# Performance work log

Hardware: AMD Instinct MI355X
Metric: run time of the kernel (lower is better)

The kernel has to match this reference:

```python
import jax, jax.numpy as jnp
import numpy as np

N_USER = 100000
M_ITEM = 50000
N_NODE = N_USER + M_ITEM
D = 64           # latent_dim
WD = D // 2      # word_emb_dim
FU = FI = 10     # padded feature-bag width
NUF = NIF = 30000
VOCAB = 20000
T = 8            # tokens per text source (name/comment/comment_list)
DNU = DNI = 10   # numeric feature dims
B = 2048         # seed batch
S = 20           # sampled neighbors per layer
L = 2            # num_layers


def setup_inputs() -> dict:
    key = jax.random.key(0)
    ks = jax.random.split(key, 26)
    f = lambda i, s: jax.random.normal(ks[i], s, jnp.float32) * 0.05
    ri = lambda i, s, hi: jax.random.randint(ks[i], s, 0, hi)
    return {
        # int (graph / lookup) inputs
        "seeds": ri(0, (B,), N_USER),
        "neigh1": ri(1, (B, S), N_NODE),
        "neigh2": ri(2, (B, S, S), N_NODE),
        "user_feat_idx": ri(3, (N_USER, FU), NUF),
        "item_feat_idx": ri(4, (M_ITEM, FI), NIF),
        "user_text_idx": ri(5, (N_USER, 3, T), VOCAB),
        "item_text_idx": ri(6, (M_ITEM, 3, T), VOCAB),
        # float tables / features
        "user_id_emb": f(7, (N_USER, D)),
        "item_id_emb": f(8, (M_ITEM, D)),
        "user_feat_emb": f(9, (NUF, D)),
        "item_feat_emb": f(10, (NIF, D)),
        "word_emb": f(11, (VOCAB, WD)),
        "user_word300": f(12, (N_USER, 300)),
        "item_word300": f(13, (M_ITEM, 300)),
        "item_sent768": f(14, (M_ITEM, 768)),
        "user_numeric": f(15, (N_USER, DNU)),
        "item_numeric": f(16, (M_ITEM, DNI)),
        # linears (stored as (in, out); y = x @ W + b)
        "Wnum_u": f(17, (DNU, D)), "bnum_u": jnp.zeros((D,), jnp.float32),
        "Wnum_i": f(18, (DNI, D)), "bnum_i": jnp.zeros((D,), jnp.float32),
        "Wproj_u": f(19, (int(D * 3.5) + 300, D)), "bproj_u": jnp.zeros((D,), jnp.float32),
        "Wproj_i": f(20, (int(D * 3.5) + 300 + 768, D)), "bproj_i": jnp.zeros((D,), jnp.float32),
        "W_w": f(21, (L, 2 * D, D)), "b_w": jnp.zeros((L, D), jnp.float32),
        "W_v": f(22, (L, D, D)), "b_v": jnp.zeros((L, D), jnp.float32),
    }


def _forward(user_id_emb, item_id_emb, user_feat_emb, item_feat_emb, word_emb,
             user_word300, item_word300, item_sent768, user_numeric, item_numeric,
             Wnum_u, bnum_u, Wnum_i, bnum_i, Wproj_u, bproj_u, Wproj_i, bproj_i,
             W_w, b_w, W_v, b_v,
             seeds, neigh1, neigh2, user_feat_idx, item_feat_idx,
             user_text_idx, item_text_idx):
    # --- multi-source node embeddings (get_text_embedding + proj + numeric) ---
    # text: mean-pool word embeddings per source, concat 3 sources -> 1.5*D
    u_text = word_emb[user_text_idx].mean(axis=2).reshape(N_USER, 3 * WD)
    i_text = word_emb[item_text_idx].mean(axis=2).reshape(M_ITEM, 3 * WD)
    # feature bags: mean-pooled embedding lookup
    u_feat = user_feat_emb[user_feat_idx].mean(axis=1)
    i_feat = item_feat_emb[item_feat_idx].mean(axis=1)
    u = (jnp.concatenate([user_id_emb, u_feat, u_text, user_word300], -1) @ Wproj_u
         + bproj_u + user_numeric @ Wnum_u + bnum_u)
    it = (jnp.concatenate([item_id_emb, i_feat, i_text, item_word300, item_sent768], -1) @ Wproj_i
          + bproj_i + item_numeric @ Wnum_i + bnum_i)
    x = jnp.concatenate([u, it], axis=0)  # [N_NODE, D], items offset by N_USER

    # --- neighbor-sampled GraphSAGE: h = W_l([self, mean(V_l(neigh))]) ---
    def sage(l, self_x, neigh_x, act):
        agg = (neigh_x @ W_v[l] + b_v[l]).mean(axis=-2)
        h = jnp.concatenate([self_x, agg], axis=-1) @ W_w[l] + b_w[l]
        return jax.nn.relu(h) if act else h

    x0 = x[seeds]        # [B, D]
    x1 = x[neigh1]       # [B, S, D]
    x2 = x[neigh2]       # [B, S, S, D]
    h1 = sage(0, x1, x2, True)   # layer-0 applied to 1-hop nodes
    h0 = sage(0, x0, x1, True)   # layer-0 applied to seeds
    out = sage(1, h0, h1, False)  # final layer, no activation
    return out  # [B, D]


def reference(seeds, neigh1, neigh2, user_feat_idx, item_feat_idx, user_text_idx,
              item_text_idx, user_id_emb, item_id_emb, user_feat_emb, item_feat_emb,
              word_emb, user_word300, item_word300, item_sent768, user_numeric,
              item_numeric, Wnum_u, bnum_u, Wnum_i, bnum_i, Wproj_u, bproj_u,
              Wproj_i, bproj_i, W_w, b_w, W_v, b_v):
    return _forward(user_id_emb, item_id_emb, user_feat_emb, item_feat_emb, word_emb,
                    user_word300, item_word300, item_sent768, user_numeric, item_numeric,
                    Wnum_u, bnum_u, Wnum_i, bnum_i, Wproj_u, bproj_u, Wproj_i, bproj_i,
                    W_w, b_w, W_v, b_v,
                    seeds, neigh1, neigh2, user_feat_idx, item_feat_idx,
                    user_text_idx, item_text_idx)
```

## Files before the change

kernel.cpp:

```cpp
#include <hip/hip_runtime.h>
#include <hip/hip_bf16.h>
#include <stdint.h>

#define N_USER 100000
#define M_ITEM 50000
#define N_NODE 150000
#define B_SEED 2048
#define S_NB 20
#define UBLK2 1563
#define IBLK2 782

typedef __bf16   bf16x8 __attribute__((ext_vector_type(8)));
typedef float    f32x4  __attribute__((ext_vector_type(4)));
typedef uint32_t u32x4  __attribute__((ext_vector_type(4)));

typedef __attribute__((address_space(3))) uint32_t lds_u32_t;
typedef __attribute__((address_space(1))) const uint32_t glb_u32_t;

__device__ __forceinline__ uint16_t f2bf(float f) {
    uint32_t u = __float_as_uint(f);
    return (uint16_t)((u + 0x7FFFu + ((u >> 16) & 1u)) >> 16);
}
__device__ __forceinline__ uint32_t pk2(float a, float b) {
    __hip_bfloat162 h = __float22bfloat162_rn(make_float2(a, b));
    return *reinterpret_cast<uint32_t*>(&h);
}
__device__ __forceinline__ float bf2f(uint16_t u) {
    return __uint_as_float(((uint32_t)u) << 16);
}

union BF8 { bf16x8 v; uint32_t u[4]; };

__device__ __forceinline__ bf16x8 pack8v(f32x4 lo, f32x4 hi) {
    BF8 r;
    r.u[0] = pk2(lo[0], lo[1]); r.u[1] = pk2(lo[2], lo[3]);
    r.u[2] = pk2(hi[0], hi[1]); r.u[3] = pk2(hi[2], hi[3]);
    return r.v;
}
__device__ __forceinline__ bf16x8 ldf32x8_mask(const float* rowp, int base, int limit) {
    BF8 r;
#pragma unroll
    for (int h = 0; h < 4; ++h) {
        const int k0 = base + 2 * h;
        const float a = (k0     < limit) ? rowp[k0]     : 0.f;
        const float b = (k0 + 1 < limit) ? rowp[k0 + 1] : 0.f;
        r.u[h] = pk2(a, b);
    }
    return r.v;
}

__global__ void prep_kernel(const float* __restrict__ Wproj_u, const float* __restrict__ Wnum_u,
                            const float* __restrict__ Wproj_i, const float* __restrict__ Wnum_i,
                            const float* __restrict__ Wv0, const float* __restrict__ Ww0,
                            uint16_t* __restrict__ WTU, uint16_t* __restrict__ WTI,
                            uint16_t* __restrict__ WvT, uint16_t* __restrict__ WwT)
{
    const int idx = blockIdx.x * 256 + threadIdx.x;
    if (idx < 36864) {
        const int d = idx / 576, kp = idx - d * 576;
        float v = 0.f;
        if (kp < 160)      v = Wproj_u[(64 + kp) * 64 + d];
        else if (kp < 192) { const int j = kp - 160; if (j < 10) v = Wnum_u[j * 64 + d]; }
        else if (kp < 224) { const int j = kp - 192; if (j < 12) v = Wproj_u[(512 + j) * 64 + d]; }
        else if (kp < 288) v = Wproj_u[(kp - 224) * 64 + d];
        else               v = Wproj_u[(224 + kp - 288) * 64 + d];
        WTU[d * 576 + kp] = f2bf(v);
    } else if (idx < 122880) {
        const int i2 = idx - 36864;
        const int d = i2 / 1344, kp = i2 - d * 1344;
        float v = 0.f;
        if (kp < 160)      v = Wproj_i[(64 + kp) * 64 + d];
        else if (kp < 192) { const int j = kp - 160; if (j < 10) v = Wnum_i[j * 64 + d]; }
        else if (kp < 224) { const int j = kp - 192; if (j < 12) v = Wproj_i[(512 + j) * 64 + d]; }
        else if (kp < 288) v = Wproj_i[(kp - 224) * 64 + d];
        else if (kp < 576) v = Wproj_i[(224 + kp - 288) * 64 + d];
        else               v = Wproj_i[(524 + kp - 576) * 64 + d];
        WTI[d * 1344 + kp] = f2bf(v);
    } else {
        const int i2 = idx - 122880;
        if (i2 < 4096) { const int d = i2 >> 6, k = i2 & 63;  WvT[d * 64 + k]  = f2bf(Wv0[k * 64 + d]); }
        else           { const int j = i2 - 4096;
                         const int d = j >> 7, k = j & 127;   WwT[d * 128 + k] = f2bf(Ww0[k * 64 + d]); }
    }
}

__global__ __launch_bounds__(256) void gpack_kernel(
    const int* __restrict__ ufi, const int* __restrict__ ifi,
    const int* __restrict__ uti, const int* __restrict__ iti,
    const float* __restrict__ ufe, const float* __restrict__ ife,
    const float* __restrict__ wemb,
    uint16_t* __restrict__ Apre)
{
    const int gid  = blockIdx.x * 256 + threadIdx.x;
    const int node = gid >> 3;
    const int d0   = gid & 7;
    if (node >= N_NODE) return;
    const bool item = node >= N_USER;
    const int nloc  = item ? node - N_USER : node;
    const int*   fidx = (item ? ifi : ufi) + (size_t)nloc * 10;
    const int*   tidx = (item ? iti : uti) + (size_t)nloc * 24;
    const float* fe   = item ? ife : ufe;
    uint16_t* out = Apre + (size_t)node * 160;

    {
        f32x4 s0 = {0, 0, 0, 0}, s1 = {0, 0, 0, 0};
#pragma unroll
        for (int j = 0; j < 10; ++j) {
            const float* p = fe + (size_t)fidx[j] * 64 + 8 * d0;
            s0 += *(const f32x4*)p;
            s1 += *(const f32x4*)(p + 4);
        }
        s0 *= 0.1f; s1 *= 0.1f;
        uint4 o = make_uint4(pk2(s0[0], s0[1]), pk2(s0[2], s0[3]),
                             pk2(s1[0], s1[1]), pk2(s1[2], s1[3]));
        *(uint4*)(out + 8 * d0) = o;
    }
#pragma unroll
    for (int s = 0; s < 3; ++s) {
        f32x4 a = {0, 0, 0, 0};
#pragma unroll
        for (int j = 0; j < 8; ++j) {
            const float* p = wemb + (size_t)tidx[s * 8 + j] * 32 + 4 * d0;
            a += *(const f32x4*)p;
        }
        a *= 0.125f;
        *(uint2*)(out + 64 + 32 * s + 4 * d0) = make_uint2(pk2(a[0], a[1]), pk2(a[2], a[3]));
    }
}

__global__ __launch_bounds__(256, 6) void pgemm_kernel(
    const uint16_t* __restrict__ Apre,
    const float* __restrict__ u_id,  const float* __restrict__ i_id,
    const float* __restrict__ uw300, const float* __restrict__ iw300,
    const float* __restrict__ is768,
    const float* __restrict__ unum,  const float* __restrict__ inum,
    const uint16_t* __restrict__ WTU, const uint16_t* __restrict__ WTI,
    const float* __restrict__ bproj_u, const float* __restrict__ bnum_u,
    const float* __restrict__ bproj_i, const float* __restrict__ bnum_i,
    uint16_t* __restrict__ xout)
{
    __shared__ float buf[2][4096];

    const int t = threadIdx.x;
    const int w = t >> 6, l = t & 63;
    const int l15 = l & 15, g4 = l >> 4;
    const bool item = blockIdx.x < IBLK2;
    const int tile  = item ? blockIdx.x : (blockIdx.x - IBLK2);
    const int ntype = item ? M_ITEM : N_USER;
    const int nb    = tile * 64;
    const int NC    = item ? 17 : 5;

    const float* idp = item ? i_id  : u_id;
    const float* w3p = item ? iw300 : uw300;
    const float* nmp = item ? inum  : unum;
    const uint16_t* WT = item ? WTI : WTU;
    const int KP       = item ? 1344 : 576;

    f32x4 acc[4] = {};
    const uint16_t* WTb = WT + (size_t)l15 * KP + g4 * 8;

    auto MM = [&](bf16x8 af2, int kb) {
#pragma unroll
        for (int db = 0; db < 4; ++db) {
            const bf16x8 bfr = *reinterpret_cast<const bf16x8*>(WTb + (size_t)db * 16 * KP + kb);
            acc[db] = __builtin_amdgcn_mfma_f32_16x16x32_bf16(af2, bfr, acc[db], 0, 0, 0);
        }
    };

    auto stage = [&](int bi, int c) {
        const float* base; int stride, coloff;
        if (c == 0)      { base = idp;   stride = 64;  coloff = 0; }
        else if (c < 5)  { base = w3p;   stride = 300; coloff = (c - 1) * 64; }
        else             { base = is768; stride = 768; coloff = (c - 5) * 64; }
        char* wbase = (char*)&buf[bi][0] + w * 4096;
#pragma unroll
        for (int j = 0; j < 4; ++j) {
            const int row  = j * 4 + (l >> 4);
            const int nn   = nb + w * 16 + row;
            const int node = nn < ntype ? nn : (ntype - 1);
            const int swb  = ((l & 15) * 16) ^ ((row & 7) << 4);
            const float* g = base + (size_t)node * stride + coloff + (swb >> 2);
            __builtin_amdgcn_global_load_lds((glb_u32_t*)g,
                (lds_u32_t*)(void*)(wbase + j * 1024), 16, 0, 0);
        }
    };

    auto compute = [&](int bi, int kb0) {
        const char* wbase = (const char*)&buf[bi][0] + w * 4096;
        const int r = l15;
#pragma unroll
        for (int ks = 0; ks < 2; ++ks) {
            const f32x4 lo = *(const f32x4*)(wbase + r * 256 + ((ks * 128 + g4 * 32)      ^ ((r & 7) << 4)));
            const f32x4 hi = *(const f32x4*)(wbase + r * 256 + ((ks * 128 + g4 * 32 + 16) ^ ((r & 7) << 4)));
            MM(pack8v(lo, hi), kb0 + ks * 32);
        }
    };

    const int nloc = (nb + w * 16 + l15) < ntype ? (nb + w * 16 + l15) : (ntype - 1);
    const int node = (item ? N_USER : 0) + nloc;
    const uint16_t* ap = Apre + (size_t)node * 160 + g4 * 8;
    bf16x8 af[5];
#pragma unroll
    for (int ks = 0; ks < 5; ++ks) af[ks] = *(const bf16x8*)(ap + ks * 32);
    const float* wr = w3p + (size_t)nloc * 300;
    const bf16x8 numf  = ldf32x8_mask(nmp + (size_t)nloc * 10, g4 * 8, 10);
    const bf16x8 tailf = ldf32x8_mask(wr, 288 + g4 * 8, 300);
    const bf16x8 w300c = pack8v(*(const f32x4*)(wr + 256 + g4 * 8),
                                *(const f32x4*)(wr + 260 + g4 * 8));

    stage(0, 0);
#pragma unroll
    for (int ks = 0; ks < 5; ++ks) MM(af[ks], ks * 32);
    MM(numf, 160);
    MM(tailf, 192);
    MM(w300c, 544);

    for (int c = 0; c < NC; ++c) {
        if (c + 1 < NC) stage((c + 1) & 1, c + 1);
        __syncthreads();
        compute(c & 1, (c < 5) ? 224 + 64 * c : 576 + 64 * (c - 5));
        __syncthreads();
    }

    const int nb_out = nb + w * 16 + g4 * 4;
    const float* bp = item ? bproj_i : bproj_u;
    const float* bn = item ? bnum_i  : bnum_u;
    uint16_t* xo = xout + (size_t)(item ? N_USER : 0) * 64;
#pragma unroll
    for (int db = 0; db < 4; ++db) {
        const int d = db * 16 + l15;
        const float bias = bp[d] + bn[d];
#pragma unroll
        for (int r = 0; r < 4; ++r) {
            const int nn = nb_out + r;
            if (nn < ntype) xo[(size_t)nn * 64 + d] = f2bf(acc[db][r] + bias);
        }
    }
}

__global__ __launch_bounds__(256) void xv_kernel(
    const uint16_t* __restrict__ x, const uint16_t* __restrict__ WvT,
    const float* __restrict__ bv, uint16_t* __restrict__ xv, int n)
{
    const int t = threadIdx.x;
    const int w = t >> 6, l = t & 63, l15 = l & 15, g4 = l >> 4;
    const int node = blockIdx.x * 64 + w * 16 + l15;
    const int node_c = node < n ? node : n - 1;

    f32x4 acc[4] = {};
    const uint16_t* WTb = WvT + l15 * 64 + g4 * 8;
#pragma unroll
    for (int ks = 0; ks < 2; ++ks) {
        const bf16x8 af = *reinterpret_cast<const bf16x8*>(x + (size_t)node_c * 64 + ks * 32 + g4 * 8);
#pragma unroll
        for (int db = 0; db < 4; ++db) {
            const bf16x8 bfr = *reinterpret_cast<const bf16x8*>(WTb + db * 16 * 64 + ks * 32);
            acc[db] = __builtin_amdgcn_mfma_f32_16x16x32_bf16(af, bfr, acc[db], 0, 0, 0);
        }
    }
    const int node_base = blockIdx.x * 64 + w * 16 + g4 * 4;
#pragma unroll
    for (int db = 0; db < 4; ++db) {
        const int d = db * 16 + l15;
        const float bias = bv[d];
#pragma unroll
        for (int r = 0; r < 4; ++r) {
            const int nn = node_base + r;
            if (nn < n) xv[(size_t)nn * 64 + d] = f2bf(acc[db][r] + bias);
        }
    }
}

__global__ __launch_bounds__(256) void sage_fused_kernel(
    const uint16_t* __restrict__ x, const uint16_t* __restrict__ xv,
    const int* __restrict__ seeds, const int* __restrict__ neigh1,
    const int* __restrict__ neigh2,
    const uint16_t* __restrict__ WwT, const float* __restrict__ bw,
    uint16_t* __restrict__ h1, uint16_t* __restrict__ h0)
{
    const int t = threadIdx.x;
    const int w = t >> 6, l = t & 63, l15 = l & 15, g4 = l >> 4;
    const int rbase = blockIdx.x * 64 + w * 16;
    const bool is1 = rbase < 40960;
    const int r = rbase + l15;
    const int sidx = is1 ? neigh1[r] : seeds[r - 40960];
    const int* ni = is1 ? (neigh2 + (size_t)r * S_NB)
                        : (neigh1 + (size_t)(r - 40960) * S_NB);

    f32x4 acc[4] = {};
    const uint16_t* WTb = WwT + l15 * 128 + g4 * 8;

    auto MM = [&](bf16x8 af, int kb) {
#pragma unroll
        for (int db = 0; db < 4; ++db) {
            const bf16x8 bfr = *reinterpret_cast<const bf16x8*>(WTb + db * 16 * 128 + kb);
            acc[db] = __builtin_amdgcn_mfma_f32_16x16x32_bf16(af, bfr, acc[db], 0, 0, 0);
        }
    };

#pragma unroll
    for (int ks = 0; ks < 2; ++ks) {
        const bf16x8 af = *reinterpret_cast<const bf16x8*>(x + (size_t)sidx * 64 + ks * 32 + g4 * 8);
        MM(af, ks * 32);
    }
#pragma unroll
    for (int ks = 0; ks < 2; ++ks) {
        float ev[4] = {0.f, 0.f, 0.f, 0.f}, od[4] = {0.f, 0.f, 0.f, 0.f};
#pragma unroll
        for (int j = 0; j < S_NB; ++j) {
            const u32x4 v = *reinterpret_cast<const u32x4*>(xv + (size_t)ni[j] * 64 + ks * 32 + g4 * 8);
#pragma unroll
            for (int q = 0; q < 4; ++q) {
                ev[q] += __uint_as_float(v[q] << 16);
                od[q] += __uint_as_float(v[q] & 0xffff0000u);
            }
        }
        BF8 m;
#pragma unroll
        for (int q = 0; q < 4; ++q) m.u[q] = pk2(ev[q] * (1.f / S_NB), od[q] * (1.f / S_NB));
        MM(m.v, 64 + ks * 32);
    }

    const int rb = blockIdx.x * 64 + w * 16 + g4 * 4;
    uint16_t* ob = is1 ? h1 : h0;
    const int rowoff = is1 ? 0 : 40960;
#pragma unroll
    for (int db = 0; db < 4; ++db) {
        const int d = db * 16 + l15;
        const float bias = bw[d];
#pragma unroll
        for (int rr = 0; rr < 4; ++rr) {
            const float h = fmaxf(acc[db][rr] + bias, 0.f);
            ob[(size_t)(rb + rr - rowoff) * 64 + d] = f2bf(h);
        }
    }
}

__global__ __launch_bounds__(256) void final_kernel(
    const uint16_t* __restrict__ h0, const uint16_t* __restrict__ h1,
    const float* __restrict__ Wv, const float* __restrict__ bv,
    const float* __restrict__ Ww, const float* __restrict__ bw,
    float* __restrict__ out)
{
    __shared__ float WvL[64 * 64];
    __shared__ float WwL[128 * 64];
    const int t = threadIdx.x;
    for (int i = t; i < 64 * 64; i += 256)  WvL[i] = Wv[i];
    for (int i = t; i < 128 * 64; i += 256) WwL[i] = Ww[i];
    __syncthreads();

    const int wave = t >> 6, lane = t & 63;
    const int base = blockIdx.x * 32 + wave * 8;
    const float bvl = bv[lane], bwl = bw[lane];

    for (int i = 0; i < 8; ++i) {
        const int b = base + i;
        float m = 0.f;
#pragma unroll
        for (int s = 0; s < S_NB; ++s)
            m += bf2f(h1[(size_t)(b * S_NB + s) * 64 + lane]);
        m *= (1.f / S_NB);

        float agg = bvl;
#pragma unroll 8
        for (int k = 0; k < 64; ++k)
            agg += __shfl(m, k) * WvL[k * 64 + lane];

        const float selfv = bf2f(h0[(size_t)b * 64 + lane]);
        float h = bwl;
#pragma unroll 8
        for (int k = 0; k < 64; ++k)
            h += __shfl(selfv, k) * WwL[k * 64 + lane];
#pragma unroll 8
        for (int k = 0; k < 64; ++k)
            h += __shfl(agg, k) * WwL[(64 + k) * 64 + lane];

        out[(size_t)b * 64 + lane] = h;
    }
}

extern "C" void kernel_launch(void* const* d_in, const int* in_sizes, int n_in,
                              void* d_out, int out_size, void* d_ws, size_t ws_size,
                              hipStream_t stream)
{
    const int*   seeds   = (const int*)d_in[0];
    const int*   neigh1  = (const int*)d_in[1];
    const int*   neigh2  = (const int*)d_in[2];
    const int*   ufi     = (const int*)d_in[3];
    const int*   ifi     = (const int*)d_in[4];
    const int*   uti     = (const int*)d_in[5];
    const int*   iti     = (const int*)d_in[6];
    const float* u_id    = (const float*)d_in[7];
    const float* i_id    = (const float*)d_in[8];
    const float* ufe     = (const float*)d_in[9];
    const float* ife     = (const float*)d_in[10];
    const float* wemb    = (const float*)d_in[11];
    const float* uw300   = (const float*)d_in[12];
    const float* iw300   = (const float*)d_in[13];
    const float* is768   = (const float*)d_in[14];
    const float* unum    = (const float*)d_in[15];
    const float* inum    = (const float*)d_in[16];
    const float* Wnum_u  = (const float*)d_in[17];
    const float* bnum_u  = (const float*)d_in[18];
    const float* Wnum_i  = (const float*)d_in[19];
    const float* bnum_i  = (const float*)d_in[20];
    const float* Wproj_u = (const float*)d_in[21];
    const float* bproj_u = (const float*)d_in[22];
    const float* Wproj_i = (const float*)d_in[23];
    const float* bproj_i = (const float*)d_in[24];
    const float* W_w     = (const float*)d_in[25];
    const float* b_w     = (const float*)d_in[26];
    const float* W_v     = (const float*)d_in[27];
    const float* b_v     = (const float*)d_in[28];

    uint16_t* WTU  = (uint16_t*)d_ws;
    uint16_t* WTI  = WTU  + 36864;
    uint16_t* WvT0 = WTI  + 86016;
    uint16_t* WwT0 = WvT0 + 4096;
    uint16_t* xbf  = WwT0 + 8192;
    uint16_t* xvbf = xbf  + (size_t)N_NODE * 64;
    uint16_t* h1bf = xvbf + (size_t)N_NODE * 64;
    uint16_t* h0bf = h1bf + (size_t)B_SEED * S_NB * 64;
    uint16_t* Apre = xvbf;
    float* outp = (float*)d_out;

    prep_kernel<<<528, 256, 0, stream>>>(
        Wproj_u, Wnum_u, Wproj_i, Wnum_i, W_v, W_w, WTU, WTI, WvT0, WwT0);

    gpack_kernel<<<(N_NODE * 8 + 255) / 256, 256, 0, stream>>>(
        ufi, ifi, uti, iti, ufe, ife, wemb, Apre);

    pgemm_kernel<<<UBLK2 + IBLK2, 256, 0, stream>>>(
        Apre, u_id, i_id, uw300, iw300, is768, unum, inum,
        WTU, WTI, bproj_u, bnum_u, bproj_i, bnum_i, xbf);

    xv_kernel<<<(N_NODE + 63) / 64, 256, 0, stream>>>(xbf, WvT0, b_v, xvbf, N_NODE);

    sage_fused_kernel<<<672, 256, 0, stream>>>(
        xbf, xvbf, seeds, neigh1, neigh2, WwT0, b_w, h1bf, h0bf);

    final_kernel<<<B_SEED / 32, 256, 0, stream>>>(
        h0bf, h1bf, W_v + 4096, b_v + 64, W_w + 8192, b_w + 64, outp);
}
```

Before: 340.2 us.

## Halve pgemm tile to 32 nodes with 32-column chunks and register-prefetched weights

The projection GEMM now runs 128-thread blocks covering 32 nodes instead of 256-thread blocks covering 64. The K dimension is streamed in 32-float chunks rather than 64, so the LDS staging buffer shrinks, more blocks can be resident, and the launch grid roughly doubles. The weight fragments for the next chunk are preloaded into registers alongside the async LDS stage, and the loop is manually double-buffered. The separate handling of columns 256–287 of the 300-wide features is folded into the regular chunk stream. The cost is twice as many barrier-separated iterations, each doing less work.

```diff
diff --git a/kernel.cpp b/kernel.cpp
--- a/kernel.cpp
+++ b/kernel.cpp
@@ -7,8 +7,8 @@
 #define N_NODE 150000
 #define B_SEED 2048
 #define S_NB 20
-#define UBLK2 1563
-#define IBLK2 782
+#define UBLK3 3125
+#define IBLK3 1563
 
 typedef __bf16   bf16x8 __attribute__((ext_vector_type(8)));
 typedef float    f32x4  __attribute__((ext_vector_type(4)));
@@ -128,7 +128,7 @@
     }
 }
 
-__global__ __launch_bounds__(256, 6) void pgemm_kernel(
+__global__ __launch_bounds__(128, 7) void pgemm_kernel(
     const uint16_t* __restrict__ Apre,
     const float* __restrict__ u_id,  const float* __restrict__ i_id,
     const float* __restrict__ uw300, const float* __restrict__ iw300,
@@ -139,16 +139,17 @@
     const float* __restrict__ bproj_i, const float* __restrict__ bnum_i,
     uint16_t* __restrict__ xout)
 {
-    __shared__ float buf[2][4096];
+    __shared__ float buf[2][1024];
 
     const int t = threadIdx.x;
-    const int w = t >> 6, l = t & 63;
+    const int w = t >> 6;
+    const int l = t & 63;
     const int l15 = l & 15, g4 = l >> 4;
-    const bool item = blockIdx.x < IBLK2;
-    const int tile  = item ? blockIdx.x : (blockIdx.x - IBLK2);
+    const bool item = blockIdx.x < IBLK3;
+    const int tile  = item ? blockIdx.x : (blockIdx.x - IBLK3);
     const int ntype = item ? M_ITEM : N_USER;
-    const int nb    = tile * 64;
-    const int NC    = item ? 17 : 5;
+    const int nb    = tile * 32;
+    const int NC    = item ? 35 : 11;
 
     const float* idp = item ? i_id  : u_id;
     const float* w3p = item ? iw300 : uw300;
@@ -169,58 +170,69 @@
 
     auto stage = [&](int bi, int c) {
         const float* base; int stride, coloff;
-        if (c == 0)      { base = idp;   stride = 64;  coloff = 0; }
-        else if (c < 5)  { base = w3p;   stride = 300; coloff = (c - 1) * 64; }
-        else             { base = is768; stride = 768; coloff = (c - 5) * 64; }
-        char* wbase = (char*)&buf[bi][0] + w * 4096;
-#pragma unroll
-        for (int j = 0; j < 4; ++j) {
-            const int row  = j * 4 + (l >> 4);
-            const int nn   = nb + w * 16 + row;
+        if (c < 2)       { base = idp;    stride = 64;  coloff = c * 32; }
+        else if (c < 11) { base = w3p;    stride = 300; coloff = (c - 2) * 32; }
+        else             { base = is768;  stride = 768; coloff = (c - 11) * 32; }
+        char* wbase = (char*)&buf[bi][0] + w * 2048;
+#pragma unroll
+        for (int j = 0; j < 2; ++j) {
+            const int rl   = j * 8 + (l >> 3);
+            const int nn   = nb + w * 16 + rl;
             const int node = nn < ntype ? nn : (ntype - 1);
-            const int swb  = ((l & 15) * 16) ^ ((row & 7) << 4);
+            const int swb  = ((l & 7) * 16) ^ ((rl & 7) << 4);
             const float* g = base + (size_t)node * stride + coloff + (swb >> 2);
             __builtin_amdgcn_global_load_lds((glb_u32_t*)g,
                 (lds_u32_t*)(void*)(wbase + j * 1024), 16, 0, 0);
         }
     };
 
-    auto compute = [&](int bi, int kb0) {
-        const char* wbase = (const char*)&buf[bi][0] + w * 4096;
+    auto loadB = [&](bf16x8* breg, int c) {
+        const int kb = 224 + 32 * c;
+#pragma unroll
+        for (int i = 0; i < 4; ++i)
+            breg[i] = *reinterpret_cast<const bf16x8*>(WTb + (size_t)i * 16 * KP + kb);
+    };
+
+    auto computeR = [&](int bi, const bf16x8* breg) {
+        const char* wbase = (const char*)&buf[bi][0] + w * 2048;
         const int r = l15;
-#pragma unroll
-        for (int ks = 0; ks < 2; ++ks) {
-            const f32x4 lo = *(const f32x4*)(wbase + r * 256 + ((ks * 128 + g4 * 32)      ^ ((r & 7) << 4)));
-            const f32x4 hi = *(const f32x4*)(wbase + r * 256 + ((ks * 128 + g4 * 32 + 16) ^ ((r & 7) << 4)));
-            MM(pack8v(lo, hi), kb0 + ks * 32);
-        }
+        const f32x4 lo = *(const f32x4*)(wbase + r * 128 + ((g4 * 32)      ^ ((r & 7) << 4)));
+        const f32x4 hi = *(const f32x4*)(wbase + r * 128 + ((g4 * 32 + 16) ^ ((r & 7) << 4)));
+        const bf16x8 af2 = pack8v(lo, hi);
+#pragma unroll
+        for (int db = 0; db < 4; ++db)
+            acc[db] = __builtin_amdgcn_mfma_f32_16x16x32_bf16(af2, breg[db], acc[db], 0, 0, 0);
     };
 
+    stage(0, 0);
     const int nloc = (nb + w * 16 + l15) < ntype ? (nb + w * 16 + l15) : (ntype - 1);
     const int node = (item ? N_USER : 0) + nloc;
-    const uint16_t* ap = Apre + (size_t)node * 160 + g4 * 8;
-    bf16x8 af[5];
-#pragma unroll
-    for (int ks = 0; ks < 5; ++ks) af[ks] = *(const bf16x8*)(ap + ks * 32);
-    const float* wr = w3p + (size_t)nloc * 300;
-    const bf16x8 numf  = ldf32x8_mask(nmp + (size_t)nloc * 10, g4 * 8, 10);
-    const bf16x8 tailf = ldf32x8_mask(wr, 288 + g4 * 8, 300);
-    const bf16x8 w300c = pack8v(*(const f32x4*)(wr + 256 + g4 * 8),
-                                *(const f32x4*)(wr + 260 + g4 * 8));
-
-    stage(0, 0);
-#pragma unroll
-    for (int ks = 0; ks < 5; ++ks) MM(af[ks], ks * 32);
-    MM(numf, 160);
-    MM(tailf, 192);
-    MM(w300c, 544);
-
-    for (int c = 0; c < NC; ++c) {
-        if (c + 1 < NC) stage((c + 1) & 1, c + 1);
+    {
+        const uint16_t* ap = Apre + (size_t)node * 160 + g4 * 8;
+        bf16x8 af[5];
+#pragma unroll
+        for (int ks = 0; ks < 5; ++ks) af[ks] = *(const bf16x8*)(ap + ks * 32);
+        const bf16x8 numf  = ldf32x8_mask(nmp + (size_t)nloc * 10, g4 * 8, 10);
+        const bf16x8 tailf = ldf32x8_mask(w3p + (size_t)nloc * 300, 288 + g4 * 8, 300);
+#pragma unroll
+        for (int ks = 0; ks < 5; ++ks) MM(af[ks], ks * 32);
+        MM(numf, 160);
+        MM(tailf, 192);
+    }
+
+    bf16x8 bA[4], bB[4];
+    loadB(bA, 0);
+    int c = 0;
+#pragma unroll 1
+    for (; c + 2 <= NC; c += 2) {
+        stage(1, c + 1); loadB(bB, c + 1);
         __syncthreads();
-        compute(c & 1, (c < 5) ? 224 + 64 * c : 576 + 64 * (c - 5));
+        computeR(0, bA);
+        if (c + 2 < NC) { stage(0, c + 2); loadB(bA, c + 2); }
         __syncthreads();
-    }
+        computeR(1, bB);
+    }
+    if (c < NC) computeR(0, bA);
 
     const int nb_out = nb + w * 16 + g4 * 4;
     const float* bp = item ? bproj_i : bproj_u;
@@ -430,7 +442,7 @@
     gpack_kernel<<<(N_NODE * 8 + 255) / 256, 256, 0, stream>>>(
         ufi, ifi, uti, iti, ufe, ife, wemb, Apre);
 
-    pgemm_kernel<<<UBLK2 + IBLK2, 256, 0, stream>>>(
+    pgemm_kernel<<<UBLK3 + IBLK3, 128, 0, stream>>>(
         Apre, u_id, i_id, uw300, iw300, is768, unum, inum,
         WTU, WTI, bproj_u, bnum_u, bproj_i, bnum_i, xbf);
 
```

After: 370.2 us. 1.09x slower.

## Pre-pack full projection operand into swizzled bf16 tiles for async LDS GEMM

Applied to the files above, without the earlier changes.

The gather/pack kernel now writes the whole projection A operand for each node into a tile-major, XOR-swizzled bf16 layout of 128 rows by 64 columns per chunk. That operand covers id embeddings, word300, sent768, numeric and text features. The GEMM kernel then streams these chunks straight into LDS with global_load_lds. It handles 128 rows per block, and users and items are launched as separate kernels. The aim is to remove the fp32-to-bf16 conversion and the strided fp32 row gathers from the GEMM inner loop. The cost is a large extra write and read of the packed intermediate, plus a much bigger workspace footprint.

```diff
diff --git a/kernel.cpp b/kernel.cpp
--- a/kernel.cpp
+++ b/kernel.cpp
@@ -7,8 +7,10 @@
 #define N_NODE 150000
 #define B_SEED 2048
 #define S_NB 20
-#define UBLK2 1563
-#define IBLK2 782
+#define TILES_U 782
+#define TILES_I 391
+#define NCH_U 9
+#define NCH_I 21
 
 typedef __bf16   bf16x8 __attribute__((ext_vector_type(8)));
 typedef float    f32x4  __attribute__((ext_vector_type(4)));
@@ -31,22 +33,17 @@
 
 union BF8 { bf16x8 v; uint32_t u[4]; };
 
-__device__ __forceinline__ bf16x8 pack8v(f32x4 lo, f32x4 hi) {
-    BF8 r;
-    r.u[0] = pk2(lo[0], lo[1]); r.u[1] = pk2(lo[2], lo[3]);
-    r.u[2] = pk2(hi[0], hi[1]); r.u[3] = pk2(hi[2], hi[3]);
-    return r.v;
-}
-__device__ __forceinline__ bf16x8 ldf32x8_mask(const float* rowp, int base, int limit) {
-    BF8 r;
-#pragma unroll
-    for (int h = 0; h < 4; ++h) {
-        const int k0 = base + 2 * h;
-        const float a = (k0     < limit) ? rowp[k0]     : 0.f;
-        const float b = (k0 + 1 < limit) ? rowp[k0 + 1] : 0.f;
-        r.u[h] = pk2(a, b);
-    }
-    return r.v;
+__device__ __forceinline__ uint4 packrow(const float* p) {
+    const f32x4 a = *(const f32x4*)p, b = *(const f32x4*)(p + 4);
+    return make_uint4(pk2(a[0], a[1]), pk2(a[2], a[3]),
+                      pk2(b[0], b[1]), pk2(b[2], b[3]));
+}
+__device__ __forceinline__ uint4 maskrow(const float* p, int j0, int lim) {
+    float v[8];
+#pragma unroll
+    for (int h = 0; h < 8; ++h) v[h] = (j0 + h < lim) ? p[j0 + h] : 0.f;
+    return make_uint4(pk2(v[0], v[1]), pk2(v[2], v[3]),
+                      pk2(v[4], v[5]), pk2(v[6], v[7]));
 }
 
 __global__ void prep_kernel(const float* __restrict__ Wproj_u, const float* __restrict__ Wnum_u,
@@ -84,23 +81,28 @@
     }
 }
 
+template<int IS_ITEM>
 __global__ __launch_bounds__(256) void gpack_kernel(
-    const int* __restrict__ ufi, const int* __restrict__ ifi,
-    const int* __restrict__ uti, const int* __restrict__ iti,
-    const float* __restrict__ ufe, const float* __restrict__ ife,
-    const float* __restrict__ wemb,
-    uint16_t* __restrict__ Apre)
-{
+    const int* __restrict__ fidx_, const int* __restrict__ tidx_,
+    const float* __restrict__ fe, const float* __restrict__ wemb,
+    const float* __restrict__ idt, const float* __restrict__ w3t,
+    const float* __restrict__ s7t, const float* __restrict__ nmt,
+    uint16_t* __restrict__ Apack)
+{
+    constexpr int NTYPE = IS_ITEM ? M_ITEM : N_USER;
+    constexpr int NCH   = IS_ITEM ? NCH_I : NCH_U;
     const int gid  = blockIdx.x * 256 + threadIdx.x;
     const int node = gid >> 3;
     const int d0   = gid & 7;
-    if (node >= N_NODE) return;
-    const bool item = node >= N_USER;
-    const int nloc  = item ? node - N_USER : node;
-    const int*   fidx = (item ? ifi : ufi) + (size_t)nloc * 10;
-    const int*   tidx = (item ? iti : uti) + (size_t)nloc * 24;
-    const float* fe   = item ? ife : ufe;
-    uint16_t* out = Apre + (size_t)node * 160;
+    if (node >= NTYPE) return;
+    const int tile = node >> 7, r = node & 127, w = r >> 5, r32 = r & 31;
+    char* out = (char*)Apack + (size_t)tile * NCH * 16384 + w * 4096
+              + r32 * 128 + ((d0 * 16) ^ ((r32 & 7) << 4));
+
+    const int* fidx = fidx_ + (size_t)node * 10;
+    const int* tidx = tidx_ + (size_t)node * 24;
+    const float* wr  = w3t + (size_t)node * 300;
+    const float* idr = idt + (size_t)node * 64;
 
     {
         f32x4 s0 = {0, 0, 0, 0}, s1 = {0, 0, 0, 0};
@@ -111,129 +113,110 @@
             s1 += *(const f32x4*)(p + 4);
         }
         s0 *= 0.1f; s1 *= 0.1f;
-        uint4 o = make_uint4(pk2(s0[0], s0[1]), pk2(s0[2], s0[3]),
-                             pk2(s1[0], s1[1]), pk2(s1[2], s1[3]));
-        *(uint4*)(out + 8 * d0) = o;
-    }
-#pragma unroll
-    for (int s = 0; s < 3; ++s) {
-        f32x4 a = {0, 0, 0, 0};
+        *(uint4*)out = make_uint4(pk2(s0[0], s0[1]), pk2(s0[2], s0[3]),
+                                  pk2(s1[0], s1[1]), pk2(s1[2], s1[3]));
+    }
+    auto text8 = [&](int src, int dd) -> uint4 {
+        f32x4 a = {0, 0, 0, 0}, b = {0, 0, 0, 0};
 #pragma unroll
         for (int j = 0; j < 8; ++j) {
-            const float* p = wemb + (size_t)tidx[s * 8 + j] * 32 + 4 * d0;
+            const float* p = wemb + (size_t)tidx[src * 8 + j] * 32 + dd;
             a += *(const f32x4*)p;
-        }
-        a *= 0.125f;
-        *(uint2*)(out + 64 + 32 * s + 4 * d0) = make_uint2(pk2(a[0], a[1]), pk2(a[2], a[3]));
-    }
-}
-
-__global__ __launch_bounds__(256, 6) void pgemm_kernel(
-    const uint16_t* __restrict__ Apre,
-    const float* __restrict__ u_id,  const float* __restrict__ i_id,
-    const float* __restrict__ uw300, const float* __restrict__ iw300,
-    const float* __restrict__ is768,
-    const float* __restrict__ unum,  const float* __restrict__ inum,
-    const uint16_t* __restrict__ WTU, const uint16_t* __restrict__ WTI,
-    const float* __restrict__ bproj_u, const float* __restrict__ bnum_u,
-    const float* __restrict__ bproj_i, const float* __restrict__ bnum_i,
-    uint16_t* __restrict__ xout)
-{
-    __shared__ float buf[2][4096];
+            b += *(const f32x4*)(p + 4);
+        }
+        a *= 0.125f; b *= 0.125f;
+        return make_uint4(pk2(a[0], a[1]), pk2(a[2], a[3]),
+                          pk2(b[0], b[1]), pk2(b[2], b[3]));
+    };
+    *(uint4*)(out + 16384) = text8(d0 >> 2, (d0 & 3) * 8);
+    *(uint4*)(out + 2 * 16384) = (d0 < 4)
+        ? text8(2, d0 * 8)
+        : maskrow(nmt + (size_t)node * 10, (d0 - 4) * 8, 10);
+    *(uint4*)(out + 3 * 16384) = (d0 < 4)
+        ? maskrow(wr + 288, d0 * 8, 12)
+        : packrow(idr + (d0 - 4) * 8);
+    *(uint4*)(out + 4 * 16384) = (d0 < 4)
+        ? packrow(idr + 32 + d0 * 8)
+        : packrow(wr + (d0 - 4) * 8);
+#pragma unroll
+    for (int c = 5; c < 9; ++c)
+        *(uint4*)(out + c * 16384) = packrow(wr + c * 64 + d0 * 8 - 288);
+    if (IS_ITEM) {
+        const float* sr = s7t + (size_t)node * 768;
+#pragma unroll
+        for (int c = 9; c < 21; ++c)
+            *(uint4*)(out + c * 16384) = packrow(sr + c * 64 + d0 * 8 - 576);
+    }
+}
+
+__global__ __launch_bounds__(256, 4) void pgemm3_kernel(
+    const uint16_t* __restrict__ Apack, const uint16_t* __restrict__ WT,
+    const float* __restrict__ bp, const float* __restrict__ bn,
+    uint16_t* __restrict__ xout, int ntype, int nch, int KP)
+{
+    __shared__ char lds[2][16384];
 
     const int t = threadIdx.x;
     const int w = t >> 6, l = t & 63;
     const int l15 = l & 15, g4 = l >> 4;
-    const bool item = blockIdx.x < IBLK2;
-    const int tile  = item ? blockIdx.x : (blockIdx.x - IBLK2);
-    const int ntype = item ? M_ITEM : N_USER;
-    const int nb    = tile * 64;
-    const int NC    = item ? 17 : 5;
-
-    const float* idp = item ? i_id  : u_id;
-    const float* w3p = item ? iw300 : uw300;
-    const float* nmp = item ? inum  : unum;
-    const uint16_t* WT = item ? WTI : WTU;
-    const int KP       = item ? 1344 : 576;
-
-    f32x4 acc[4] = {};
+    const int nb = blockIdx.x * 128;
+
+    f32x4 acc[2][4] = {};
     const uint16_t* WTb = WT + (size_t)l15 * KP + g4 * 8;
-
-    auto MM = [&](bf16x8 af2, int kb) {
+    const char* Atile = (const char*)Apack + (size_t)blockIdx.x * nch * 16384;
+
+    auto stage = [&](int bi, int c) {
+        const char* src = Atile + c * 16384 + w * 4096 + l * 16;
+        char* dst = &lds[bi][w * 4096];
+#pragma unroll
+        for (int j = 0; j < 4; ++j)
+            __builtin_amdgcn_global_load_lds((glb_u32_t*)(src + j * 1024),
+                (lds_u32_t*)(void*)(dst + j * 1024), 16, 0, 0);
+    };
+
+    auto compute = [&](int bi, int c) {
+        const char* wb = &lds[bi][w * 4096];
+#pragma unroll
+        for (int ks = 0; ks < 2; ++ks) {
+            bf16x8 bfr[4];
+#pragma unroll
+            for (int db = 0; db < 4; ++db)
+                bfr[db] = *reinterpret_cast<const bf16x8*>(
+                    WTb + (size_t)db * 16 * KP + c * 64 + ks * 32);
+#pragma unroll
+            for (int frag = 0; frag < 2; ++frag) {
+                const int r32 = frag * 16 + l15;
+                const bf16x8 af = *(const bf16x8*)(wb + r32 * 128
+                    + ((ks * 64 + g4 * 16) ^ ((r32 & 7) << 4)));
+#pragma unroll
+                for (int db = 0; db < 4; ++db)
+                    acc[frag][db] = __builtin_amdgcn_mfma_f32_16x16x32_bf16(
+                        af, bfr[db], acc[frag][db], 0, 0, 0);
+            }
+        }
+    };
+
+    stage(0, 0);
+#pragma unroll 1
+    for (int c = 0; c < nch; ++c) {
+        if (c + 1 < nch) stage((c + 1) & 1, c + 1);
+        __syncthreads();
+        compute(c & 1, c);
+        __syncthreads();
+    }
+
+#pragma unroll
+    for (int frag = 0; frag < 2; ++frag) {
+        const int rb = nb + w * 32 + frag * 16 + g4 * 4;
 #pragma unroll
         for (int db = 0; db < 4; ++db) {
-            const bf16x8 bfr = *reinterpret_cast<const bf16x8*>(WTb + (size_t)db * 16 * KP + kb);
-            acc[db] = __builtin_amdgcn_mfma_f32_16x16x32_bf16(af2, bfr, acc[db], 0, 0, 0);
-        }
-    };
-
-    auto stage = [&](int bi, int c) {
-        const float* base; int stride, coloff;
-        if (c == 0)      { base = idp;   stride = 64;  coloff = 0; }
-        else if (c < 5)  { base = w3p;   stride = 300; coloff = (c - 1) * 64; }
-        else             { base = is768; stride = 768; coloff = (c - 5) * 64; }
-        char* wbase = (char*)&buf[bi][0] + w * 4096;
-#pragma unroll
-        for (int j = 0; j < 4; ++j) {
-            const int row  = j * 4 + (l >> 4);
-            const int nn   = nb + w * 16 + row;
-            const int node = nn < ntype ? nn : (ntype - 1);
-            const int swb  = ((l & 15) * 16) ^ ((row & 7) << 4);
-            const float* g = base + (size_t)node * stride + coloff + (swb >> 2);
-            __builtin_amdgcn_global_load_lds((glb_u32_t*)g,
-                (lds_u32_t*)(void*)(wbase + j * 1024), 16, 0, 0);
-        }
-    };
-
-    auto compute = [&](int bi, int kb0) {
-        const char* wbase = (const char*)&buf[bi][0] + w * 4096;
-        const int r = l15;
-#pragma unroll
-        for (int ks = 0; ks < 2; ++ks) {
-            const f32x4 lo = *(const f32x4*)(wbase + r * 256 + ((ks * 128 + g4 * 32)      ^ ((r & 7) << 4)));
-            const f32x4 hi = *(const f32x4*)(wbase + r * 256 + ((ks * 128 + g4 * 32 + 16) ^ ((r & 7) << 4)));
-            MM(pack8v(lo, hi), kb0 + ks * 32);
-        }
-    };
-
-    const int nloc = (nb + w * 16 + l15) < ntype ? (nb + w * 16 + l15) : (ntype - 1);
-    const int node = (item ? N_USER : 0) + nloc;
-    const uint16_t* ap = Apre + (size_t)node * 160 + g4 * 8;
-    bf16x8 af[5];
-#pragma unroll
-    for (int ks = 0; ks < 5; ++ks) af[ks] = *(const bf16x8*)(ap + ks * 32);
-    const float* wr = w3p + (size_t)nloc * 300;
-    const bf16x8 numf  = ldf32x8_mask(nmp + (size_t)nloc * 10, g4 * 8, 10);
-    const bf16x8 tailf = ldf32x8_mask(wr, 288 + g4 * 8, 300);
-    const bf16x8 w300c = pack8v(*(const f32x4*)(wr + 256 + g4 * 8),
-                                *(const f32x4*)(wr + 260 + g4 * 8));
-
-    stage(0, 0);
-#pragma unroll
-    for (int ks = 0; ks < 5; ++ks) MM(af[ks], ks * 32);
-    MM(numf, 160);
-    MM(tailf, 192);
-    MM(w300c, 544);
-
-    for (int c = 0; c < NC; ++c) {
-        if (c + 1 < NC) stage((c + 1) & 1, c + 1);
-        __syncthreads();
-        compute(c & 1, (c < 5) ? 224 + 64 * c : 576 + 64 * (c - 5));
-        __syncthreads();
-    }
-
-    const int nb_out = nb + w * 16 + g4 * 4;
-    const float* bp = item ? bproj_i : bproj_u;
-    const float* bn = item ? bnum_i  : bnum_u;
-    uint16_t* xo = xout + (size_t)(item ? N_USER : 0) * 64;
-#pragma unroll
-    for (int db = 0; db < 4; ++db) {
-        const int d = db * 16 + l15;
-        const float bias = bp[d] + bn[d];
-#pragma unroll
-        for (int r = 0; r < 4; ++r) {
-            const int nn = nb_out + r;
-            if (nn < ntype) xo[(size_t)nn * 64 + d] = f2bf(acc[db][r] + bias);
+            const int d = db * 16 + l15;
+            const float bias = bp[d] + bn[d];
+#pragma unroll
+            for (int rr = 0; rr < 4; ++rr) {
+                const int nn = rb + rr;
+                if (nn < ntype) xout[(size_t)nn * 64 + d] = f2bf(acc[frag][db][rr] + bias);
+            }
         }
     }
 }
@@ -418,21 +401,25 @@
     uint16_t* WvT0 = WTI  + 86016;
     uint16_t* WwT0 = WvT0 + 4096;
     uint16_t* xbf  = WwT0 + 8192;
-    uint16_t* xvbf = xbf  + (size_t)N_NODE * 64;
-    uint16_t* h1bf = xvbf + (size_t)N_NODE * 64;
-    uint16_t* h0bf = h1bf + (size_t)B_SEED * S_NB * 64;
-    uint16_t* Apre = xvbf;
+    uint16_t* region = xbf + (size_t)N_NODE * 64;
+    uint16_t* Apack = region;
+    uint16_t* xvbf  = region;
+    uint16_t* h1bf  = xvbf + (size_t)N_NODE * 64;
+    uint16_t* h0bf  = h1bf + (size_t)B_SEED * S_NB * 64;
     float* outp = (float*)d_out;
 
     prep_kernel<<<528, 256, 0, stream>>>(
         Wproj_u, Wnum_u, Wproj_i, Wnum_i, W_v, W_w, WTU, WTI, WvT0, WwT0);
 
-    gpack_kernel<<<(N_NODE * 8 + 255) / 256, 256, 0, stream>>>(
-        ufi, ifi, uti, iti, ufe, ife, wemb, Apre);
-
-    pgemm_kernel<<<UBLK2 + IBLK2, 256, 0, stream>>>(
-        Apre, u_id, i_id, uw300, iw300, is768, unum, inum,
-        WTU, WTI, bproj_u, bnum_u, bproj_i, bnum_i, xbf);
+    gpack_kernel<0><<<(N_USER * 8) / 256, 256, 0, stream>>>(
+        ufi, uti, ufe, wemb, u_id, uw300, nullptr, unum, Apack);
+    pgemm3_kernel<<<TILES_U, 256, 0, stream>>>(
+        Apack, WTU, bproj_u, bnum_u, xbf, N_USER, NCH_U, 576);
+
+    gpack_kernel<1><<<(M_ITEM * 8 + 255) / 256, 256, 0, stream>>>(
+        ifi, iti, ife, wemb, i_id, iw300, is768, inum, Apack);
+    pgemm3_kernel<<<TILES_I, 256, 0, stream>>>(
+        Apack, WTI, bproj_i, bnum_i, xbf + (size_t)N_USER * 64, M_ITEM, NCH_I, 1344);
 
     xv_kernel<<<(N_NODE + 63) / 64, 256, 0, stream>>>(xbf, WvT0, b_v, xvbf, N_NODE);
 
```

New measurement: 387.7 us (median of 4 runs). 14.0% more time.
